# Optimization experiments

Hardware: AMD Instinct MI355X
Metric: run time of the kernel (lower is better)

The kernel has to match this reference:

```python
import jax, jax.numpy as jnp
import numpy as np

D_MODEL = 1024
NUM_HEADS = 16
D_K = D_MODEL // NUM_HEADS


def setup_inputs() -> dict:
    key = jax.random.key(0)
    ks = jax.random.split(key, 9)
    s = 1.0 / np.sqrt(D_MODEL)
    x = jax.random.normal(ks[0], (2, 2048, D_MODEL), dtype=jnp.float32)
    Wq = jax.random.uniform(ks[1], (D_MODEL, D_MODEL), jnp.float32, -s, s)
    bq = jax.random.uniform(ks[2], (D_MODEL,), jnp.float32, -s, s)
    Wk = jax.random.uniform(ks[3], (D_MODEL, D_MODEL), jnp.float32, -s, s)
    bk = jax.random.uniform(ks[4], (D_MODEL,), jnp.float32, -s, s)
    Wv = jax.random.uniform(ks[5], (D_MODEL, D_MODEL), jnp.float32, -s, s)
    bv = jax.random.uniform(ks[6], (D_MODEL,), jnp.float32, -s, s)
    Wo = jax.random.uniform(ks[7], (D_MODEL, D_MODEL), jnp.float32, -s, s)
    bo = jax.random.uniform(ks[8], (D_MODEL,), jnp.float32, -s, s)
    return {"x": x, "Wq": Wq, "bq": bq, "Wk": Wk, "bk": bk,
            "Wv": Wv, "bv": bv, "Wo": Wo, "bo": bo}


def reference(x, Wq, bq, Wk, bk, Wv, bv, Wo, bo):
    B, S, _ = x.shape
    # projections (torch Linear: x @ W.T + b; here W stored as [in, out])
    q = (x @ Wq + bq).reshape(B, S, NUM_HEADS, D_K).transpose(0, 2, 1, 3)
    k = (x @ Wk + bk).reshape(B, S, NUM_HEADS, D_K).transpose(0, 2, 1, 3)
    v = (x @ Wv + bv).reshape(B, S, NUM_HEADS, D_K).transpose(0, 2, 1, 3)
    scores = jnp.einsum('bhqd,bhkd->bhqk', q, k) / jnp.sqrt(jnp.float32(D_K))
    attn = jax.nn.softmax(scores, axis=-1)
    out = jnp.einsum('bhqk,bhkd->bhqd', attn, v)  # [B,H,S,Dk]
    out = out.transpose(0, 2, 1, 3).reshape(B, S, D_MODEL)
    return out @ Wo + bo
```

## Files before the change

### kernel.cpp

```cpp
#include <hip/hip_runtime.h>
#include <hip/hip_bf16.h>

#define SEQ   2048
#define DM    1024
#define NH    16
#define DK    64
#define BATCH 2
#define M_TOT 4096
#define C1 0.18033688011112042f

typedef __attribute__((ext_vector_type(8))) short bf16x8;
typedef __attribute__((ext_vector_type(4))) float f32x4;
typedef unsigned short u16;

__device__ inline u16 f2b(float f) {
    union { float f; unsigned u; } x; x.f = f;
    return (u16)((x.u + 0x7FFFu + ((x.u >> 16) & 1u)) >> 16);
}

__device__ inline unsigned pk2(float a, float b) {
    __hip_bfloat162 h = __float22bfloat162_rn(make_float2(a, b));
    return *reinterpret_cast<unsigned*>(&h);
}

__device__ inline void async_cp16(const u16* g, u16* l) {
    __builtin_amdgcn_global_load_lds(
        (const __attribute__((address_space(1))) unsigned int*)g,
        (__attribute__((address_space(3))) unsigned int*)l, 16, 0, 0);
}

__global__ __launch_bounds__(256) void cast_x(
    const float4* __restrict__ x, uint2* __restrict__ xb)
{
    int gid = blockIdx.x * 256 + threadIdx.x;
    float4 v = x[gid];
    uint2 o;
    o.x = pk2(v.x, v.y); o.y = pk2(v.z, v.w);
    xb[gid] = o;
}

__global__ __launch_bounds__(256) void transpose_cast4(
    const float* __restrict__ W0, const float* __restrict__ W1,
    const float* __restrict__ W2, const float* __restrict__ W3,
    u16* __restrict__ WtBase)
{
    __shared__ float tile[32][33];
    const int t = threadIdx.x;
    const int n0 = blockIdx.x << 5, k0 = blockIdx.y << 5, z = blockIdx.z;
    const float* W = (z == 0) ? W0 : (z == 1) ? W1 : (z == 2) ? W2 : W3;
    u16* Wt = WtBase + (size_t)z * DM * DM;
    #pragma unroll
    for (int i = 0; i < 4; ++i) {
        int idx = t + (i << 8); int r = idx >> 5, c = idx & 31;
        tile[r][c] = W[(size_t)(k0 + r) * DM + n0 + c];
    }
    __syncthreads();
    #pragma unroll
    for (int i = 0; i < 4; ++i) {
        int idx = t + (i << 8); int r = idx >> 5, c = idx & 31;
        Wt[(size_t)(n0 + r) * DM + k0 + c] = f2b(tile[c][r]);
    }
}

__global__ __launch_bounds__(256) void gemm_bt(
    const u16* __restrict__ A, const u16* __restrict__ Bt, int mode,
    const float* __restrict__ bias0, const float* __restrict__ bias1,
    const float* __restrict__ bias2,
    void* __restrict__ out0, void* __restrict__ out1, void* __restrict__ out2)
{
    __shared__ u16 sh[9216];
    u16* As = sh;
    u16* Bs = sh + 4096;
    const int t = threadIdx.x, wid = t >> 6, lane = t & 63;
    const int lr = lane & 15, quad = lane >> 4;
    const int m0 = blockIdx.y << 7, n0 = blockIdx.x << 7;
    const int wm = (wid & 1) << 6, wn = (wid >> 1) << 6;
    const int rowA = lane >> 2;
    const int colA = (((lane & 3) - ((lane >> 3) & 3)) & 3) << 3;
    const int sA = (((lr >> 1) + quad) & 3) << 3;

    f32x4 acc[4][4];
    #pragma unroll
    for (int i = 0; i < 4; ++i)
        #pragma unroll
        for (int j = 0; j < 4; ++j) acc[i][j] = (f32x4){0.f, 0.f, 0.f, 0.f};

    for (int k0 = 0; k0 < DM; k0 += 32) {
        #pragma unroll
        for (int i = 0; i < 2; ++i) {
            int ch = wid * 2 + i;
            async_cp16(A  + (size_t)(m0 + ch * 16 + rowA) * DM + k0 + colA,
                       As + ch * 16 * 32);
            async_cp16(Bt + (size_t)(n0 + ch * 16 + rowA) * DM + k0 + colA,
                       Bs + ch * 16 * 32);
        }
        __syncthreads();
        bf16x8 af[4], bfr[4];
        #pragma unroll
        for (int mt = 0; mt < 4; ++mt)
            af[mt] = *(const bf16x8*)(As + (wm + 16 * mt + lr) * 32 + sA);
        #pragma unroll
        for (int nt = 0; nt < 4; ++nt)
            bfr[nt] = *(const bf16x8*)(Bs + (wn + 16 * nt + lr) * 32 + sA);
        #pragma unroll
        for (int mt = 0; mt < 4; ++mt)
            #pragma unroll
            for (int nt = 0; nt < 4; ++nt)
                acc[mt][nt] = __builtin_amdgcn_mfma_f32_16x16x32_bf16(
                    af[mt], bfr[nt], acc[mt][nt], 0, 0, 0);
        __syncthreads();
    }

    if (mode == 1) {
        u16* wstrip = sh + wid * 1152;
        const int ngb = n0 + wn;
        const int which = ngb >> 10, nnb = ngb & 1023;
        const int h = nnb >> 6;
        const float* bp = (which == 0) ? bias0 : (which == 1) ? bias1 : bias2;
        const float sc = (which == 0) ? C1 : 1.0f;
        float bias_v[4];
        #pragma unroll
        for (int nt = 0; nt < 4; ++nt) bias_v[nt] = bp[nnb + 16 * nt + lr];

        if (which != 1) {
            u16* dst = (which == 0) ? (u16*)out0 : (u16*)out2;
            #pragma unroll
            for (int mt = 0; mt < 4; ++mt) {
                #pragma unroll
                for (int nt = 0; nt < 4; ++nt) {
                    uint2 w;
                    w.x = pk2((acc[mt][nt][0] + bias_v[nt]) * sc,
                              (acc[mt][nt][1] + bias_v[nt]) * sc);
                    w.y = pk2((acc[mt][nt][2] + bias_v[nt]) * sc,
                              (acc[mt][nt][3] + bias_v[nt]) * sc);
                    *(uint2*)(wstrip + (16 * nt + lr) * 16 + quad * 4) = w;
                }
                asm volatile("s_waitcnt lgkmcnt(0)" ::: "memory");
                #pragma unroll
                for (int half = 0; half < 2; ++half) {
                    int id = lane + 64 * half;
                    int d = id >> 1, cho = (id & 1) << 3;
                    int m = m0 + wm + 16 * mt + cho;
                    int b = m >> 11, s = m & (SEQ - 1);
                    *(uint4*)(dst + ((size_t)(b * NH + h) * DK + d) * SEQ + s) =
                        *(const uint4*)(wstrip + d * 16 + cho);
                }
                asm volatile("s_waitcnt lgkmcnt(0)" ::: "memory");
            }
        } else {
            u16* dst = (u16*)out1;
            #pragma unroll
            for (int mt = 0; mt < 4; ++mt) {
                #pragma unroll
                for (int nt = 0; nt < 4; ++nt)
                    #pragma unroll
                    for (int r = 0; r < 4; ++r)
                        wstrip[(quad * 4 + r) * 72 + 16 * nt + lr] =
                            f2b(acc[mt][nt][r] + bias_v[nt]);
                asm volatile("s_waitcnt lgkmcnt(0)" ::: "memory");
                #pragma unroll
                for (int half = 0; half < 2; ++half) {
                    int id = lane + 64 * half;
                    int mloc = id >> 3, dl = (id & 7) << 3;
                    int m = m0 + wm + 16 * mt + mloc;
                    int b = m >> 11, s = m & (SEQ - 1);
                    *(uint4*)(dst + ((size_t)(b * NH + h) * SEQ + s) * DK + dl) =
                        *(const uint4*)(wstrip + mloc * 72 + dl);
                }
                asm volatile("s_waitcnt lgkmcnt(0)" ::: "memory");
            }
        }
    } else {
        float* O = (float*)out0;
        float* strip = (float*)sh + wid * 1088;
        float bias_v[4];
        #pragma unroll
        for (int nt = 0; nt < 4; ++nt) bias_v[nt] = bias0[n0 + wn + 16 * nt + lr];
        #pragma unroll
        for (int mt = 0; mt < 4; ++mt) {
            #pragma unroll
            for (int nt = 0; nt < 4; ++nt)
                #pragma unroll
                for (int r = 0; r < 4; ++r)
                    strip[(quad * 4 + r) * 68 + 16 * nt + lr] =
                        acc[mt][nt][r] + bias_v[nt];
            asm volatile("s_waitcnt lgkmcnt(0)" ::: "memory");
            #pragma unroll
            for (int rr = 0; rr < 4; ++rr) {
                int row = lane >> 2, chunk = (lane & 3) + 4 * rr;
                float4 v = *(const float4*)(strip + row * 68 + chunk * 4);
                *(float4*)(O + (size_t)(m0 + wm + 16 * mt + row) * DM
                             + n0 + wn + chunk * 4) = v;
            }
            asm volatile("s_waitcnt lgkmcnt(0)" ::: "memory");
        }
    }
}

__global__ __launch_bounds__(256) void attn_mfma(
    const u16* __restrict__ Qt, const u16* __restrict__ K,
    const u16* __restrict__ Vt, u16* __restrict__ A)
{
    __shared__ u16 sh[20480];

    const int t = threadIdx.x, wid = t >> 6, lane = t & 63;
    const int lr = lane & 15, quad = lane >> 4;
    const int bx = blockIdx.x;
    const int xcd = bx & 7, within = bx >> 3;
    const int bh  = xcd * 4 + (within >> 5);
    const int q0  = (within & 31) << 6;

    const u16* Kb = K  + (size_t)bh * SEQ * DK;
    const u16* Vb = Vt + (size_t)bh * DK * SEQ;

    const int q = q0 + 16 * wid + lr;
    const u16* Qb = Qt + (size_t)bh * DK * SEQ + q;
    bf16x8 bQ0, bQ1;
    #pragma unroll
    for (int j = 0; j < 8; ++j) {
        bQ0[j] = (short)Qb[(size_t)(quad * 8 + j) * SEQ];
        bQ1[j] = (short)Qb[(size_t)(32 + quad * 8 + j) * SEQ];
    }

    f32x4 O[4];
    #pragma unroll
    for (int mt = 0; mt < 4; ++mt) O[mt] = (f32x4){0.f, 0.f, 0.f, 0.f};
    float l_r = 0.f;

    const int srow = t >> 3, schunk = t & 7;
    const int sslot = ((schunk ^ (srow & 7)) << 3);
    const int soff0 = srow * 64 + sslot;
    const int soff1 = (srow + 32) * 64 + sslot;
    const int c0 = ((quad ^ (lr & 7)) << 3);
    const int c1 = (((quad + 4) ^ (lr & 7)) << 3);
    const int prow = 16384 + (16 * wid + lr) * 64;

    uint4 kr0 = *(const uint4*)(Kb + (size_t)srow * DK + schunk * 8);
    uint4 kr1 = *(const uint4*)(Kb + (size_t)(srow + 32) * DK + schunk * 8);
    uint4 vr0 = *(const uint4*)(Vb + (size_t)srow * SEQ + schunk * 8);
    uint4 vr1 = *(const uint4*)(Vb + (size_t)(srow + 32) * SEQ + schunk * 8);
    *(uint4*)(sh + soff0) = kr0;
    *(uint4*)(sh + soff1) = kr1;
    *(uint4*)(sh + 8192 + soff0) = vr0;
    *(uint4*)(sh + 8192 + soff1) = vr1;
    kr0 = *(const uint4*)(Kb + (size_t)(64 + srow) * DK + schunk * 8);
    kr1 = *(const uint4*)(Kb + (size_t)(64 + srow + 32) * DK + schunk * 8);
    vr0 = *(const uint4*)(Vb + (size_t)srow * SEQ + 64 + schunk * 8);
    vr1 = *(const uint4*)(Vb + (size_t)(srow + 32) * SEQ + 64 + schunk * 8);
    __syncthreads();

    for (int it = 0; it < SEQ / 64; ++it) {
        const int kbase = (it & 1) << 12;
        const int vbase = 8192 + ((it & 1) << 12);

        f32x4 S[4];
        #pragma unroll
        for (int mt = 0; mt < 4; ++mt) {
            bf16x8 a0 = *(const bf16x8*)(sh + kbase + (16 * mt + lr) * 64 + c0);
            bf16x8 a1 = *(const bf16x8*)(sh + kbase + (16 * mt + lr) * 64 + c1);
            f32x4 s = (f32x4){0.f, 0.f, 0.f, 0.f};
            s = __builtin_amdgcn_mfma_f32_16x16x32_bf16(a0, bQ0, s, 0, 0, 0);
            s = __builtin_amdgcn_mfma_f32_16x16x32_bf16(a1, bQ1, s, 0, 0, 0);
            S[mt] = s;
        }

        #pragma unroll
        for (int mt = 0; mt < 4; ++mt) {
            float e0 = __builtin_amdgcn_exp2f(S[mt][0]);
            float e1 = __builtin_amdgcn_exp2f(S[mt][1]);
            float e2 = __builtin_amdgcn_exp2f(S[mt][2]);
            float e3 = __builtin_amdgcn_exp2f(S[mt][3]);
            l_r += (e0 + e1) + (e2 + e3);
            uint2 pk;
            pk.x = pk2(e0, e1); pk.y = pk2(e2, e3);
            int chunk = 2 * mt + (quad >> 1);
            *(uint2*)(sh + prow + ((chunk ^ (lr & 7)) << 3)
                         + ((quad & 1) << 2)) = pk;
        }
        asm volatile("s_waitcnt lgkmcnt(0)" ::: "memory");

        bf16x8 p0 = *(const bf16x8*)(sh + prow + c0);
        bf16x8 p1 = *(const bf16x8*)(sh + prow + c1);
        #pragma unroll
        for (int mt = 0; mt < 4; ++mt) {
            bf16x8 v0 = *(const bf16x8*)(sh + vbase + (16 * mt + lr) * 64 + c0);
            bf16x8 v1 = *(const bf16x8*)(sh + vbase + (16 * mt + lr) * 64 + c1);
            O[mt] = __builtin_amdgcn_mfma_f32_16x16x32_bf16(v0, p0, O[mt], 0, 0, 0);
            O[mt] = __builtin_amdgcn_mfma_f32_16x16x32_bf16(v1, p1, O[mt], 0, 0, 0);
        }

        if (it < SEQ / 64 - 1) {
            const int kn = ((it + 1) & 1) << 12;
            const int vn = 8192 + (((it + 1) & 1) << 12);
            *(uint4*)(sh + kn + soff0) = kr0;
            *(uint4*)(sh + kn + soff1) = kr1;
            *(uint4*)(sh + vn + soff0) = vr0;
            *(uint4*)(sh + vn + soff1) = vr1;
            if (it < SEQ / 64 - 2) {
                int nt2 = (it + 2) * 64;
                kr0 = *(const uint4*)(Kb + (size_t)(nt2 + srow) * DK + schunk * 8);
                kr1 = *(const uint4*)(Kb + (size_t)(nt2 + srow + 32) * DK + schunk * 8);
                vr0 = *(const uint4*)(Vb + (size_t)srow * SEQ + nt2 + schunk * 8);
                vr1 = *(const uint4*)(Vb + (size_t)(srow + 32) * SEQ + nt2 + schunk * 8);
            }
            __syncthreads();
        }
    }

    l_r += __shfl_xor(l_r, 16);
    l_r += __shfl_xor(l_r, 32);

    const int b = bh >> 4, h = bh & 15;
    float inv = 1.f / l_r;
    #pragma unroll
    for (int mt = 0; mt < 4; ++mt) {
        uint2 pk;
        pk.x = pk2(O[mt][0] * inv, O[mt][1] * inv);
        pk.y = pk2(O[mt][2] * inv, O[mt][3] * inv);
        *(uint2*)(A + (size_t)(b * SEQ + q) * DM + h * DK + 16 * mt + 4 * quad) = pk;
    }
}

extern "C" void kernel_launch(void* const* d_in, const int* in_sizes, int n_in,
                              void* d_out, int out_size, void* d_ws, size_t ws_size,
                              hipStream_t stream)
{
    const float* x  = (const float*)d_in[0];
    const float* Wq = (const float*)d_in[1];
    const float* bq = (const float*)d_in[2];
    const float* Wk = (const float*)d_in[3];
    const float* bk = (const float*)d_in[4];
    const float* Wv = (const float*)d_in[5];
    const float* bv = (const float*)d_in[6];
    const float* Wo = (const float*)d_in[7];
    const float* bo = (const float*)d_in[8];

    const size_t NE = (size_t)M_TOT * DM;
    u16* xb     = (u16*)d_ws;
    u16* wt_qkv = xb + NE;
    u16* wt_o   = wt_qkv + 3 * (size_t)DM * DM;
    u16* qt_ws  = wt_o + (size_t)DM * DM;
    u16* k_ws   = qt_ws + NE;
    u16* vt_ws  = k_ws + NE;
    u16* a_ws   = vt_ws + NE;

    cast_x<<<M_TOT * DM / 4 / 256, 256, 0, stream>>>((const float4*)x, (uint2*)xb);
    transpose_cast4<<<dim3(32, 32, 4), 256, 0, stream>>>(Wq, Wk, Wv, Wo, wt_qkv);

    gemm_bt<<<dim3(24, 32), 256, 0, stream>>>(
        xb, wt_qkv, 1, bq, bk, bv, qt_ws, k_ws, vt_ws);

    attn_mfma<<<dim3(1024), 256, 0, stream>>>(qt_ws, k_ws, vt_ws, a_ws);

    gemm_bt<<<dim3(8, 32), 256, 0, stream>>>(
        a_ws, wt_o, 0, bo, nullptr, nullptr, d_out, nullptr, nullptr);
}
```

Baseline: 217.1 us.

## Process 128 queries per attention block and stage K/V with async copies

Each wave now handles two 16-query groups, so every K/V fragment read from shared memory feeds twice as many MFMAs. The block covers 128 queries and the grid halves to 512 blocks. The register-staged K/V prefetch is replaced by direct global-to-LDS async copies into a double buffer, issued at the top of each iteration. This roughly halves K/V global and LDS traffic per query, at the cost of more registers, more LDS, and fewer blocks to fill the GPU.

```diff
diff --git a/kernel.cpp b/kernel.cpp
--- a/kernel.cpp
+++ b/kernel.cpp
@@ -201,123 +201,119 @@
     const u16* __restrict__ Qt, const u16* __restrict__ K,
     const u16* __restrict__ Vt, u16* __restrict__ A)
 {
-    __shared__ u16 sh[20480];
+    __shared__ u16 sh[24576];
 
     const int t = threadIdx.x, wid = t >> 6, lane = t & 63;
     const int lr = lane & 15, quad = lane >> 4;
     const int bx = blockIdx.x;
     const int xcd = bx & 7, within = bx >> 3;
-    const int bh  = xcd * 4 + (within >> 5);
-    const int q0  = (within & 31) << 6;
+    const int bh  = xcd * 4 + (within >> 4);
+    const int q0  = (within & 15) << 7;
 
     const u16* Kb = K  + (size_t)bh * SEQ * DK;
     const u16* Vb = Vt + (size_t)bh * DK * SEQ;
 
-    const int q = q0 + 16 * wid + lr;
-    const u16* Qb = Qt + (size_t)bh * DK * SEQ + q;
-    bf16x8 bQ0, bQ1;
-    #pragma unroll
-    for (int j = 0; j < 8; ++j) {
-        bQ0[j] = (short)Qb[(size_t)(quad * 8 + j) * SEQ];
-        bQ1[j] = (short)Qb[(size_t)(32 + quad * 8 + j) * SEQ];
-    }
-
-    f32x4 O[4];
-    #pragma unroll
-    for (int mt = 0; mt < 4; ++mt) O[mt] = (f32x4){0.f, 0.f, 0.f, 0.f};
-    float l_r = 0.f;
-
-    const int srow = t >> 3, schunk = t & 7;
-    const int sslot = ((schunk ^ (srow & 7)) << 3);
-    const int soff0 = srow * 64 + sslot;
-    const int soff1 = (srow + 32) * 64 + sslot;
+    const int qbase = q0 + 32 * wid + lr;
+    const u16* Qb = Qt + (size_t)bh * DK * SEQ;
+    bf16x8 bQ[2][2];
+    #pragma unroll
+    for (int g = 0; g < 2; ++g) {
+        const u16* Qp = Qb + qbase + 16 * g;
+        #pragma unroll
+        for (int j = 0; j < 8; ++j) {
+            bQ[g][0][j] = (short)Qp[(size_t)(quad * 8 + j) * SEQ];
+            bQ[g][1][j] = (short)Qp[(size_t)(32 + quad * 8 + j) * SEQ];
+        }
+    }
+
+    f32x4 O[2][4];
+    #pragma unroll
+    for (int g = 0; g < 2; ++g)
+        #pragma unroll
+        for (int mt = 0; mt < 4; ++mt) O[g][mt] = (f32x4){0.f, 0.f, 0.f, 0.f};
+    float l_r[2] = {0.f, 0.f};
+
+    const int srow = t >> 3;
+    const int scol = (((t & 7) ^ (srow & 7)) << 3);
+
     const int c0 = ((quad ^ (lr & 7)) << 3);
     const int c1 = (((quad + 4) ^ (lr & 7)) << 3);
-    const int prow = 16384 + (16 * wid + lr) * 64;
-
-    uint4 kr0 = *(const uint4*)(Kb + (size_t)srow * DK + schunk * 8);
-    uint4 kr1 = *(const uint4*)(Kb + (size_t)(srow + 32) * DK + schunk * 8);
-    uint4 vr0 = *(const uint4*)(Vb + (size_t)srow * SEQ + schunk * 8);
-    uint4 vr1 = *(const uint4*)(Vb + (size_t)(srow + 32) * SEQ + schunk * 8);
-    *(uint4*)(sh + soff0) = kr0;
-    *(uint4*)(sh + soff1) = kr1;
-    *(uint4*)(sh + 8192 + soff0) = vr0;
-    *(uint4*)(sh + 8192 + soff1) = vr1;
-    kr0 = *(const uint4*)(Kb + (size_t)(64 + srow) * DK + schunk * 8);
-    kr1 = *(const uint4*)(Kb + (size_t)(64 + srow + 32) * DK + schunk * 8);
-    vr0 = *(const uint4*)(Vb + (size_t)srow * SEQ + 64 + schunk * 8);
-    vr1 = *(const uint4*)(Vb + (size_t)(srow + 32) * SEQ + 64 + schunk * 8);
+    const int prow = 16384 + wid * 2048 + lr * 64;
+
+    auto stage = [&](int kt, int buf) {
+        u16* kd = sh + (buf << 12);
+        u16* vd = sh + 8192 + (buf << 12);
+        async_cp16(Kb + (size_t)(kt + srow) * DK + scol,       kd + wid * 512);
+        async_cp16(Kb + (size_t)(kt + srow + 32) * DK + scol,  kd + 2048 + wid * 512);
+        async_cp16(Vb + (size_t)srow * SEQ + kt + scol,        vd + wid * 512);
+        async_cp16(Vb + (size_t)(srow + 32) * SEQ + kt + scol, vd + 2048 + wid * 512);
+    };
+
+    stage(0, 0);
     __syncthreads();
 
     for (int it = 0; it < SEQ / 64; ++it) {
         const int kbase = (it & 1) << 12;
         const int vbase = 8192 + ((it & 1) << 12);
-
-        f32x4 S[4];
+        if (it + 1 < SEQ / 64) stage((it + 1) << 6, (it + 1) & 1);
+
         #pragma unroll
         for (int mt = 0; mt < 4; ++mt) {
             bf16x8 a0 = *(const bf16x8*)(sh + kbase + (16 * mt + lr) * 64 + c0);
             bf16x8 a1 = *(const bf16x8*)(sh + kbase + (16 * mt + lr) * 64 + c1);
-            f32x4 s = (f32x4){0.f, 0.f, 0.f, 0.f};
-            s = __builtin_amdgcn_mfma_f32_16x16x32_bf16(a0, bQ0, s, 0, 0, 0);
-            s = __builtin_amdgcn_mfma_f32_16x16x32_bf16(a1, bQ1, s, 0, 0, 0);
-            S[mt] = s;
-        }
-
-        #pragma unroll
-        for (int mt = 0; mt < 4; ++mt) {
-            float e0 = __builtin_amdgcn_exp2f(S[mt][0]);
-            float e1 = __builtin_amdgcn_exp2f(S[mt][1]);
-            float e2 = __builtin_amdgcn_exp2f(S[mt][2]);
-            float e3 = __builtin_amdgcn_exp2f(S[mt][3]);
-            l_r += (e0 + e1) + (e2 + e3);
-            uint2 pk;
-            pk.x = pk2(e0, e1); pk.y = pk2(e2, e3);
-            int chunk = 2 * mt + (quad >> 1);
-            *(uint2*)(sh + prow + ((chunk ^ (lr & 7)) << 3)
-                         + ((quad & 1) << 2)) = pk;
+            #pragma unroll
+            for (int g = 0; g < 2; ++g) {
+                f32x4 s = (f32x4){0.f, 0.f, 0.f, 0.f};
+                s = __builtin_amdgcn_mfma_f32_16x16x32_bf16(a0, bQ[g][0], s, 0, 0, 0);
+                s = __builtin_amdgcn_mfma_f32_16x16x32_bf16(a1, bQ[g][1], s, 0, 0, 0);
+                float e0 = __builtin_amdgcn_exp2f(s[0]);
+                float e1 = __builtin_amdgcn_exp2f(s[1]);
+                float e2 = __builtin_amdgcn_exp2f(s[2]);
+                float e3 = __builtin_amdgcn_exp2f(s[3]);
+                l_r[g] += (e0 + e1) + (e2 + e3);
+                uint2 pk;
+                pk.x = pk2(e0, e1); pk.y = pk2(e2, e3);
+                int chunk = 2 * mt + (quad >> 1);
+                *(uint2*)(sh + prow + (g << 10) + ((chunk ^ (lr & 7)) << 3)
+                             + ((quad & 1) << 2)) = pk;
+            }
         }
         asm volatile("s_waitcnt lgkmcnt(0)" ::: "memory");
 
-        bf16x8 p0 = *(const bf16x8*)(sh + prow + c0);
-        bf16x8 p1 = *(const bf16x8*)(sh + prow + c1);
+        bf16x8 p00 = *(const bf16x8*)(sh + prow + c0);
+        bf16x8 p01 = *(const bf16x8*)(sh + prow + c1);
+        bf16x8 p10 = *(const bf16x8*)(sh + prow + 1024 + c0);
+        bf16x8 p11 = *(const bf16x8*)(sh + prow + 1024 + c1);
         #pragma unroll
         for (int mt = 0; mt < 4; ++mt) {
             bf16x8 v0 = *(const bf16x8*)(sh + vbase + (16 * mt + lr) * 64 + c0);
             bf16x8 v1 = *(const bf16x8*)(sh + vbase + (16 * mt + lr) * 64 + c1);
-            O[mt] = __builtin_amdgcn_mfma_f32_16x16x32_bf16(v0, p0, O[mt], 0, 0, 0);
-            O[mt] = __builtin_amdgcn_mfma_f32_16x16x32_bf16(v1, p1, O[mt], 0, 0, 0);
-        }
-
-        if (it < SEQ / 64 - 1) {
-            const int kn = ((it + 1) & 1) << 12;
-            const int vn = 8192 + (((it + 1) & 1) << 12);
-            *(uint4*)(sh + kn + soff0) = kr0;
-            *(uint4*)(sh + kn + soff1) = kr1;
-            *(uint4*)(sh + vn + soff0) = vr0;
-            *(uint4*)(sh + vn + soff1) = vr1;
-            if (it < SEQ / 64 - 2) {
-                int nt2 = (it + 2) * 64;
-                kr0 = *(const uint4*)(Kb + (size_t)(nt2 + srow) * DK + schunk * 8);
-                kr1 = *(const uint4*)(Kb + (size_t)(nt2 + srow + 32) * DK + schunk * 8);
-                vr0 = *(const uint4*)(Vb + (size_t)srow * SEQ + nt2 + schunk * 8);
-                vr1 = *(const uint4*)(Vb + (size_t)(srow + 32) * SEQ + nt2 + schunk * 8);
-            }
-            __syncthreads();
-        }
-    }
-
-    l_r += __shfl_xor(l_r, 16);
-    l_r += __shfl_xor(l_r, 32);
+            O[0][mt] = __builtin_amdgcn_mfma_f32_16x16x32_bf16(v0, p00, O[0][mt], 0, 0, 0);
+            O[0][mt] = __builtin_amdgcn_mfma_f32_16x16x32_bf16(v1, p01, O[0][mt], 0, 0, 0);
+            O[1][mt] = __builtin_amdgcn_mfma_f32_16x16x32_bf16(v0, p10, O[1][mt], 0, 0, 0);
+            O[1][mt] = __builtin_amdgcn_mfma_f32_16x16x32_bf16(v1, p11, O[1][mt], 0, 0, 0);
+        }
+        if (it + 1 < SEQ / 64) __syncthreads();
+    }
+
+    #pragma unroll
+    for (int g = 0; g < 2; ++g) {
+        l_r[g] += __shfl_xor(l_r[g], 16);
+        l_r[g] += __shfl_xor(l_r[g], 32);
+    }
 
     const int b = bh >> 4, h = bh & 15;
-    float inv = 1.f / l_r;
-    #pragma unroll
-    for (int mt = 0; mt < 4; ++mt) {
-        uint2 pk;
-        pk.x = pk2(O[mt][0] * inv, O[mt][1] * inv);
-        pk.y = pk2(O[mt][2] * inv, O[mt][3] * inv);
-        *(uint2*)(A + (size_t)(b * SEQ + q) * DM + h * DK + 16 * mt + 4 * quad) = pk;
+    #pragma unroll
+    for (int g = 0; g < 2; ++g) {
+        float inv = 1.f / l_r[g];
+        const int q = qbase + 16 * g;
+        #pragma unroll
+        for (int mt = 0; mt < 4; ++mt) {
+            uint2 pk;
+            pk.x = pk2(O[g][mt][0] * inv, O[g][mt][1] * inv);
+            pk.y = pk2(O[g][mt][2] * inv, O[g][mt][3] * inv);
+            *(uint2*)(A + (size_t)(b * SEQ + q) * DM + h * DK + 16 * mt + 4 * quad) = pk;
+        }
     }
 }
 
@@ -350,7 +346,7 @@
     gemm_bt<<<dim3(24, 32), 256, 0, stream>>>(
         xb, wt_qkv, 1, bq, bk, bv, qt_ws, k_ws, vt_ws);
 
-    attn_mfma<<<dim3(1024), 256, 0, stream>>>(qt_ws, k_ws, vt_ws, a_ws);
+    attn_mfma<<<dim3(512), 256, 0, stream>>>(qt_ws, k_ws, vt_ws, a_ws);
 
     gemm_bt<<<dim3(8, 32), 256, 0, stream>>>(
         a_ws, wt_o, 0, bo, nullptr, nullptr, d_out, nullptr, nullptr);
```

Result: no change. 217.3 us (+0.1%).
